# Optimization experiments

Measured on AMD Instinct MI355X. Metric: run time of the kernel, lower is better.

Reference implementation:

```python
import itertools
import jax, jax.numpy as jnp
import numpy as np

N1 = 4
N2 = 4
D = 3
BATCH = 512
NDENSE = 256
FEAT_IN = (N1 + N2) * D  # 24


def _perms_and_signs(n):
    P = np.array(list(itertools.permutations(range(n))), dtype=np.int32)  # [n!, n], lexicographic
    # sign = (-1)^(number of inversions)
    triu = np.triu(np.ones((n, n), dtype=np.int64), 1)
    inv = np.sum((P[:, :, None] > P[:, None, :]) * triu, axis=(1, 2))
    signs = np.where(inv % 2 == 0, 1.0, -1.0).astype(np.float32)
    return P, signs

P1_np, S1_np = _perms_and_signs(N1)
P2_np, S2_np = _perms_and_signs(N2)


def setup_inputs() -> dict:
    key = jax.random.key(0)
    ks = jax.random.split(key, 12)
    def dense_init(k, fan_in, fan_out):
        return jax.random.normal(k, (fan_in, fan_out), jnp.float32) / jnp.sqrt(jnp.float32(fan_in))
    inp = {
        "x1": jax.random.normal(ks[0], (BATCH, N1, D), jnp.float32),
        "x2": jax.random.normal(ks[1], (BATCH, N2, D), jnp.float32),
        "W0": dense_init(ks[2], FEAT_IN, NDENSE),
        "b0": jnp.zeros((NDENSE,), jnp.float32),
        "W1": dense_init(ks[3], NDENSE, NDENSE),
        "b1": jnp.zeros((NDENSE,), jnp.float32),
        "W2": dense_init(ks[4], NDENSE, NDENSE),
        "b2": jnp.zeros((NDENSE,), jnp.float32),
        "Wf": dense_init(ks[5], NDENSE, 1),
        "bf": jnp.zeros((1,), jnp.float32),
    }
    return inp


def _resnet(h, W0, b0, W1, b1, W2, b2, Wf, bf):
    # SimpleResNet: residual tanh dense layers (skip when shapes match), linear head
    y = jnp.tanh(h @ W0 + b0)            # [.., 24] -> [.., 256]: no skip (shape mismatch)
    y = jnp.tanh(y @ W1 + b1) + y        # residual
    y = jnp.tanh(y @ W2 + b2) + y        # residual
    return y @ Wf + bf                   # [.., 1], no activation


def reference(x1, x2, W0, b0, W1, b1, W2, b2, Wf, bf):
    P1 = jnp.asarray(P1_np); P2 = jnp.asarray(P2_np)
    s1 = jnp.asarray(S1_np); s2 = jnp.asarray(S2_np)
    nf1, nf2 = P1.shape[0], P2.shape[0]  # 24, 24
    # all permutations along particle axis
    p1 = jnp.take(x1, P1, axis=-2)       # [B, nf1, n1, d]
    p2 = jnp.take(x2, P2, axis=-2)       # [B, nf2, n2, d]
    # broadcast to cross product of permutation axes
    b1_ = jnp.broadcast_to(p1[:, :, None, :, :], (x1.shape[0], nf1, nf2, N1, D))
    b2_ = jnp.broadcast_to(p2[:, None, :, :, :], (x2.shape[0], nf1, nf2, N2, D))
    concat = jnp.concatenate([b1_, b2_], axis=-2)                  # [B, nf1, nf2, n1+n2, d]
    feats = concat.reshape(concat.shape[:-2] + (-1,))              # [B, nf1, nf2, (n1+n2)*d]
    out = _resnet(feats, W0, b0, W1, b1, W2, b2, Wf, bf)           # [B, nf1, nf2, 1]
    signed = out * s1[:, None, None] * s2[:, None]                 # sign-weighted
    anti = jnp.sum(signed, axis=(-1, -2, -3))                      # [B]
    return jnp.log(jnp.abs(anti))
```

## Files before the change

kernel.cpp:

```cpp
#include <hip/hip_runtime.h>
#include <math.h>

#define NPERM 24
#define ND 256
#define RPB 48
#define RPW 12
#define ROWS_PER_B 576
#define BATCH 512
#define TOTAL_ROWS (BATCH * ROWS_PER_B)
#define NBLOCKS (TOTAL_ROWS / RPB)

__constant__ int c_P[NPERM * 4] = {
    0,1,2,3, 0,1,3,2, 0,2,1,3, 0,2,3,1, 0,3,1,2, 0,3,2,1,
    1,0,2,3, 1,0,3,2, 1,2,0,3, 1,2,3,0, 1,3,0,2, 1,3,2,0,
    2,0,1,3, 2,0,3,1, 2,1,0,3, 2,1,3,0, 2,3,0,1, 2,3,1,0,
    3,0,1,2, 3,0,2,1, 3,1,0,2, 3,1,2,0, 3,2,0,1, 3,2,1,0
};
__constant__ float c_S[NPERM] = {
     1.f,-1.f,-1.f, 1.f, 1.f,-1.f,
    -1.f, 1.f, 1.f,-1.f,-1.f, 1.f,
     1.f,-1.f,-1.f, 1.f, 1.f,-1.f,
    -1.f, 1.f, 1.f,-1.f,-1.f, 1.f
};

__global__ __launch_bounds__(256, 2)
void fused_resnet(const float* __restrict__ x1, const float* __restrict__ x2,
                  const float* __restrict__ W0, const float* __restrict__ b0,
                  const float* __restrict__ W1, const float* __restrict__ b1,
                  const float* __restrict__ W2, const float* __restrict__ b2,
                  const float* __restrict__ Wf, const float* __restrict__ bf,
                  double* __restrict__ anti)
{
    __shared__ float sY[RPB * ND];
    __shared__ float sStage[4096];
    const int t   = threadIdx.x;
    const int tc  = t & 63;
    const int tr  = t >> 6;
    const int gr0 = blockIdx.x * RPB;
    const int b   = gr0 / ROWS_PER_B;

    for (int e = t; e < RPB * 24; e += 256) {
        int lr = e / 24, c = e % 24;
        int pp = (gr0 + lr) % ROWS_PER_B;
        float v;
        if (c < 12) {
            int p1 = pp / 24;
            v = x1[b * 12 + c_P[p1 * 4 + c / 3] * 3 + (c % 3)];
        } else {
            int p2 = pp % 24; int cc = c - 12;
            v = x2[b * 12 + c_P[p2 * 4 + cc / 3] * 3 + (cc % 3)];
        }
        sStage[2048 + e] = v;
    }

    float acc[RPW][4];

    #pragma unroll
    for (int r = 0; r < RPW; ++r) { acc[r][0]=0.f; acc[r][1]=0.f; acc[r][2]=0.f; acc[r][3]=0.f; }
    for (int kt = 0; kt < 24; kt += 8) {
        __syncthreads();
        {
            const float4* src = (const float4*)(W0 + kt * ND);
            float4* dst = (float4*)sStage;
            for (int i = t; i < (8 * ND) / 4; i += 256) dst[i] = src[i];
        }
        __syncthreads();
        #pragma unroll
        for (int k4 = 0; k4 < 2; ++k4) {
            float w[4][4];
            #pragma unroll
            for (int k = 0; k < 4; ++k) {
                float4 wv = *(const float4*)&sStage[(k4 * 4 + k) * ND + 4 * tc];
                w[k][0]=wv.x; w[k][1]=wv.y; w[k][2]=wv.z; w[k][3]=wv.w;
            }
            #pragma unroll
            for (int r = 0; r < RPW; ++r) {
                float4 yv = *(const float4*)&sStage[2048 + (tr * RPW + r) * 24 + kt + k4 * 4];
                float yk[4] = {yv.x, yv.y, yv.z, yv.w};
                #pragma unroll
                for (int k = 0; k < 4; ++k)
                    #pragma unroll
                    for (int c = 0; c < 4; ++c)
                        acc[r][c] = fmaf(yk[k], w[k][c], acc[r][c]);
            }
        }
    }
    {
        float4 bv = *(const float4*)&b0[4 * tc];
        float bb[4] = {bv.x, bv.y, bv.z, bv.w};
        __syncthreads();
        #pragma unroll
        for (int r = 0; r < RPW; ++r) {
            float4 o;
            o.x = tanhf(acc[r][0] + bb[0]);
            o.y = tanhf(acc[r][1] + bb[1]);
            o.z = tanhf(acc[r][2] + bb[2]);
            o.w = tanhf(acc[r][3] + bb[3]);
            *(float4*)&sY[(tr * RPW + r) * ND + 4 * tc] = o;
        }
        __syncthreads();
    }

    #pragma unroll 1
    for (int layer = 0; layer < 2; ++layer) {
        const float* W   = layer ? W2 : W1;
        const float* bbp = layer ? b2 : b1;
        #pragma unroll
        for (int r = 0; r < RPW; ++r) { acc[r][0]=0.f; acc[r][1]=0.f; acc[r][2]=0.f; acc[r][3]=0.f; }
        for (int kt = 0; kt < ND; kt += 16) {
            __syncthreads();
            {
                const float4* src = (const float4*)(W + kt * ND);
                float4* dst = (float4*)sStage;
                #pragma unroll
                for (int i = 0; i < 4; ++i) dst[t + i * 256] = src[t + i * 256];
            }
            __syncthreads();
            #pragma unroll
            for (int k4 = 0; k4 < 4; ++k4) {
                float w[4][4];
                #pragma unroll
                for (int k = 0; k < 4; ++k) {
                    float4 wv = *(const float4*)&sStage[(k4 * 4 + k) * ND + 4 * tc];
                    w[k][0]=wv.x; w[k][1]=wv.y; w[k][2]=wv.z; w[k][3]=wv.w;
                }
                #pragma unroll
                for (int r = 0; r < RPW; ++r) {
                    float4 yv = *(const float4*)&sY[(tr * RPW + r) * ND + kt + k4 * 4];
                    float yk[4] = {yv.x, yv.y, yv.z, yv.w};
                    #pragma unroll
                    for (int k = 0; k < 4; ++k)
                        #pragma unroll
                        for (int c = 0; c < 4; ++c)
                            acc[r][c] = fmaf(yk[k], w[k][c], acc[r][c]);
                }
            }
        }
        float4 bv = *(const float4*)&bbp[4 * tc];
        float bb[4] = {bv.x, bv.y, bv.z, bv.w};
        float ny[RPW][4];
        #pragma unroll
        for (int r = 0; r < RPW; ++r) {
            float4 yo = *(const float4*)&sY[(tr * RPW + r) * ND + 4 * tc];
            float yov[4] = {yo.x, yo.y, yo.z, yo.w};
            #pragma unroll
            for (int c = 0; c < 4; ++c)
                ny[r][c] = tanhf(acc[r][c] + bb[c]) + yov[c];
        }
        __syncthreads();
        #pragma unroll
        for (int r = 0; r < RPW; ++r) {
            float4 o; o.x = ny[r][0]; o.y = ny[r][1]; o.z = ny[r][2]; o.w = ny[r][3];
            *(float4*)&sY[(tr * RPW + r) * ND + 4 * tc] = o;
        }
        __syncthreads();
    }

    if (t < 64) {
        ((float4*)sStage)[t] = ((const float4*)Wf)[t];
    }
    __syncthreads();
    double contrib = 0.0;
    if (tc < RPW) {
        int row = tr * RPW + tc;
        const float* yrow = &sY[row * ND];
        float f = 0.f;
        #pragma unroll 8
        for (int k = 0; k < ND; ++k) f = fmaf(yrow[k], sStage[k], f);
        f += bf[0];
        int pp = (gr0 + row) % ROWS_PER_B;
        double s = (double)(c_S[pp / 24] * c_S[pp % 24]);
        contrib = s * (double)f;
    }
    #pragma unroll
    for (int off = 32; off > 0; off >>= 1) contrib += __shfl_xor(contrib, off, 64);
    if (tc == 0) atomicAdd(&anti[b], contrib);
}

__global__ void finalize_log(const double* __restrict__ anti, float* __restrict__ out) {
    int i = blockIdx.x * 256 + threadIdx.x;
    if (i < BATCH) out[i] = (float)log(fabs(anti[i]));
}

extern "C" void kernel_launch(void* const* d_in, const int* in_sizes, int n_in,
                              void* d_out, int out_size, void* d_ws, size_t ws_size,
                              hipStream_t stream) {
    const float* x1 = (const float*)d_in[0];
    const float* x2 = (const float*)d_in[1];
    const float* W0 = (const float*)d_in[2];
    const float* b0 = (const float*)d_in[3];
    const float* W1 = (const float*)d_in[4];
    const float* b1 = (const float*)d_in[5];
    const float* W2 = (const float*)d_in[6];
    const float* b2 = (const float*)d_in[7];
    const float* Wf = (const float*)d_in[8];
    const float* bf = (const float*)d_in[9];
    double* anti = (double*)d_ws;
    float* out   = (float*)d_out;

    hipMemsetAsync(anti, 0, BATCH * sizeof(double), stream);
    fused_resnet<<<NBLOCKS, 256, 0, stream>>>(x1, x2, W0, b0, W1, b1, W2, b2, Wf, bf, anti);
    finalize_log<<<(BATCH + 255) / 256, 256, 0, stream>>>(anti, out);
}
```

Before: 1.295 ms.

## Double-buffer weight tiles in LDS using async global_load_lds prefetch

```diff
diff --git a/kernel.cpp b/kernel.cpp
--- a/kernel.cpp
+++ b/kernel.cpp
@@ -7,8 +7,7 @@
 #define RPW 12
 #define ROWS_PER_B 576
 #define BATCH 512
-#define TOTAL_ROWS (BATCH * ROWS_PER_B)
-#define NBLOCKS (TOTAL_ROWS / RPB)
+#define NBLOCKS (BATCH * ROWS_PER_B / RPB)
 
 __constant__ int c_P[NPERM * 4] = {
     0,1,2,3, 0,1,3,2, 0,2,1,3, 0,2,3,1, 0,3,1,2, 0,3,2,1,
@@ -23,6 +22,12 @@
     -1.f, 1.f, 1.f,-1.f,-1.f, 1.f
 };
 
+__device__ __forceinline__ void gl_lds16(const float* g, float* l) {
+    __builtin_amdgcn_global_load_lds(
+        (const __attribute__((address_space(1))) void*)g,
+        (__attribute__((address_space(3)))  void*)l, 16, 0, 0);
+}
+
 __global__ __launch_bounds__(256, 2)
 void fused_resnet(const float* __restrict__ x1, const float* __restrict__ x2,
                   const float* __restrict__ W0, const float* __restrict__ b0,
@@ -32,12 +37,18 @@
                   double* __restrict__ anti)
 {
     __shared__ float sY[RPB * ND];
-    __shared__ float sStage[4096];
+    __shared__ float sW[8192];
     const int t   = threadIdx.x;
     const int tc  = t & 63;
     const int tr  = t >> 6;
     const int gr0 = blockIdx.x * RPB;
     const int b   = gr0 / ROWS_PER_B;
+
+    #pragma unroll
+    for (int i = 0; i < 2; ++i) {
+        int c = tr * 2 + i;
+        gl_lds16(W0 + c * 256 + tc * 4, &sW[c * 256]);
+    }
 
     for (int e = t; e < RPB * 24; e += 256) {
         int lr = e / 24, c = e % 24;
@@ -50,32 +61,36 @@
             int p2 = pp % 24; int cc = c - 12;
             v = x2[b * 12 + c_P[p2 * 4 + cc / 3] * 3 + (cc % 3)];
         }
-        sStage[2048 + e] = v;
+        sW[4096 + e] = v;
     }
 
     float acc[RPW][4];
 
     #pragma unroll
     for (int r = 0; r < RPW; ++r) { acc[r][0]=0.f; acc[r][1]=0.f; acc[r][2]=0.f; acc[r][3]=0.f; }
-    for (int kt = 0; kt < 24; kt += 8) {
+    for (int kt3 = 0; kt3 < 3; ++kt3) {
         __syncthreads();
-        {
-            const float4* src = (const float4*)(W0 + kt * ND);
-            float4* dst = (float4*)sStage;
-            for (int i = t; i < (8 * ND) / 4; i += 256) dst[i] = src[i];
-        }
-        __syncthreads();
+        if (kt3 < 2) {
+            const float* src = W0 + (kt3 + 1) * 2048;
+            float* dst = &sW[((kt3 + 1) & 1) * 2048];
+            #pragma unroll
+            for (int i = 0; i < 2; ++i) {
+                int c = tr * 2 + i;
+                gl_lds16(src + c * 256 + tc * 4, dst + c * 256);
+            }
+        }
+        const float* wt = &sW[(kt3 & 1) * 2048];
         #pragma unroll
         for (int k4 = 0; k4 < 2; ++k4) {
             float w[4][4];
             #pragma unroll
             for (int k = 0; k < 4; ++k) {
-                float4 wv = *(const float4*)&sStage[(k4 * 4 + k) * ND + 4 * tc];
+                float4 wv = *(const float4*)&wt[(k4 * 4 + k) * 256 + 4 * tc];
                 w[k][0]=wv.x; w[k][1]=wv.y; w[k][2]=wv.z; w[k][3]=wv.w;
             }
             #pragma unroll
             for (int r = 0; r < RPW; ++r) {
-                float4 yv = *(const float4*)&sStage[2048 + (tr * RPW + r) * 24 + kt + k4 * 4];
+                float4 yv = *(const float4*)&sW[4096 + (tr * RPW + r) * 24 + kt3 * 8 + k4 * 4];
                 float yk[4] = {yv.x, yv.y, yv.z, yv.w};
                 #pragma unroll
                 for (int k = 0; k < 4; ++k)
@@ -85,10 +100,15 @@
             }
         }
     }
+    __syncthreads();
+    #pragma unroll
+    for (int i = 0; i < 4; ++i) {
+        int c = tr * 4 + i;
+        gl_lds16(W1 + c * 256 + tc * 4, &sW[4096 + c * 256]);
+    }
     {
         float4 bv = *(const float4*)&b0[4 * tc];
         float bb[4] = {bv.x, bv.y, bv.z, bv.w};
-        __syncthreads();
         #pragma unroll
         for (int r = 0; r < RPW; ++r) {
             float4 o;
@@ -98,35 +118,47 @@
             o.w = tanhf(acc[r][3] + bb[3]);
             *(float4*)&sY[(tr * RPW + r) * ND + 4 * tc] = o;
         }
-        __syncthreads();
-    }
-
+    }
+
+    int cur = 1;
     #pragma unroll 1
     for (int layer = 0; layer < 2; ++layer) {
-        const float* W   = layer ? W2 : W1;
-        const float* bbp = layer ? b2 : b1;
+        const float* Wcur = layer ? W2 : W1;
+        const float* bcur = layer ? b2 : b1;
         #pragma unroll
         for (int r = 0; r < RPW; ++r) { acc[r][0]=0.f; acc[r][1]=0.f; acc[r][2]=0.f; acc[r][3]=0.f; }
-        for (int kt = 0; kt < ND; kt += 16) {
+        #pragma unroll 1
+        for (int ktile = 0; ktile < 16; ++ktile) {
             __syncthreads();
-            {
-                const float4* src = (const float4*)(W + kt * ND);
-                float4* dst = (float4*)sStage;
-                #pragma unroll
-                for (int i = 0; i < 4; ++i) dst[t + i * 256] = src[t + i * 256];
-            }
-            __syncthreads();
+            float* nb = &sW[(1 - cur) * 4096];
+            if (ktile < 15) {
+                const float* src = Wcur + (ktile + 1) * 4096;
+                #pragma unroll
+                for (int i = 0; i < 4; ++i) {
+                    int c = tr * 4 + i;
+                    gl_lds16(src + c * 256 + tc * 4, nb + c * 256);
+                }
+            } else if (layer == 0) {
+                #pragma unroll
+                for (int i = 0; i < 4; ++i) {
+                    int c = tr * 4 + i;
+                    gl_lds16(W2 + c * 256 + tc * 4, nb + c * 256);
+                }
+            } else {
+                gl_lds16(Wf + tc * 4, nb + tr * 256);
+            }
+            const float* wt = &sW[cur * 4096];
             #pragma unroll
             for (int k4 = 0; k4 < 4; ++k4) {
                 float w[4][4];
                 #pragma unroll
                 for (int k = 0; k < 4; ++k) {
-                    float4 wv = *(const float4*)&sStage[(k4 * 4 + k) * ND + 4 * tc];
+                    float4 wv = *(const float4*)&wt[(k4 * 4 + k) * 256 + 4 * tc];
                     w[k][0]=wv.x; w[k][1]=wv.y; w[k][2]=wv.z; w[k][3]=wv.w;
                 }
                 #pragma unroll
                 for (int r = 0; r < RPW; ++r) {
-                    float4 yv = *(const float4*)&sY[(tr * RPW + r) * ND + kt + k4 * 4];
+                    float4 yv = *(const float4*)&sY[(tr * RPW + r) * ND + ktile * 16 + k4 * 4];
                     float yk[4] = {yv.x, yv.y, yv.z, yv.w};
                     #pragma unroll
                     for (int k = 0; k < 4; ++k)
@@ -135,38 +167,31 @@
                             acc[r][c] = fmaf(yk[k], w[k][c], acc[r][c]);
                 }
             }
-        }
-        float4 bv = *(const float4*)&bbp[4 * tc];
+            cur ^= 1;
+        }
+        float4 bv = *(const float4*)&bcur[4 * tc];
         float bb[4] = {bv.x, bv.y, bv.z, bv.w};
-        float ny[RPW][4];
         #pragma unroll
         for (int r = 0; r < RPW; ++r) {
             float4 yo = *(const float4*)&sY[(tr * RPW + r) * ND + 4 * tc];
-            float yov[4] = {yo.x, yo.y, yo.z, yo.w};
-            #pragma unroll
-            for (int c = 0; c < 4; ++c)
-                ny[r][c] = tanhf(acc[r][c] + bb[c]) + yov[c];
-        }
-        __syncthreads();
-        #pragma unroll
-        for (int r = 0; r < RPW; ++r) {
-            float4 o; o.x = ny[r][0]; o.y = ny[r][1]; o.z = ny[r][2]; o.w = ny[r][3];
+            float4 o;
+            o.x = tanhf(acc[r][0] + bb[0]) + yo.x;
+            o.y = tanhf(acc[r][1] + bb[1]) + yo.y;
+            o.z = tanhf(acc[r][2] + bb[2]) + yo.z;
+            o.w = tanhf(acc[r][3] + bb[3]) + yo.w;
             *(float4*)&sY[(tr * RPW + r) * ND + 4 * tc] = o;
         }
-        __syncthreads();
-    }
-
-    if (t < 64) {
-        ((float4*)sStage)[t] = ((const float4*)Wf)[t];
-    }
+    }
+
     __syncthreads();
     double contrib = 0.0;
     if (tc < RPW) {
         int row = tr * RPW + tc;
         const float* yrow = &sY[row * ND];
+        const float* wfp  = &sW[4096 + tr * 256];
         float f = 0.f;
         #pragma unroll 8
-        for (int k = 0; k < ND; ++k) f = fmaf(yrow[k], sStage[k], f);
+        for (int k = 0; k < ND; ++k) f = fmaf(yrow[k], wfp[k], f);
         f += bf[0];
         int pp = (gr0 + row) % ROWS_PER_B;
         double s = (double)(c_S[pp / 24] * c_S[pp % 24]);
```

Result: slower. 1.483 ms (+14.5%).

## Assign one row per lane with wave-uniform weight columns read via scalar loads

Applied to the files above, without the earlier changes.

```diff
diff --git a/kernel.cpp b/kernel.cpp
--- a/kernel.cpp
+++ b/kernel.cpp
@@ -1,22 +1,20 @@
 #include <hip/hip_runtime.h>
 #include <math.h>
 
-#define NPERM 24
 #define ND 256
-#define RPB 48
-#define RPW 12
+#define RPB 64
 #define ROWS_PER_B 576
 #define BATCH 512
-#define TOTAL_ROWS (BATCH * ROWS_PER_B)
-#define NBLOCKS (TOTAL_ROWS / RPB)
+#define BPE 9
+#define NBLOCKS (BATCH * BPE)
 
-__constant__ int c_P[NPERM * 4] = {
+__constant__ int c_P[24 * 4] = {
     0,1,2,3, 0,1,3,2, 0,2,1,3, 0,2,3,1, 0,3,1,2, 0,3,2,1,
     1,0,2,3, 1,0,3,2, 1,2,0,3, 1,2,3,0, 1,3,0,2, 1,3,2,0,
     2,0,1,3, 2,0,3,1, 2,1,0,3, 2,1,3,0, 2,3,0,1, 2,3,1,0,
     3,0,1,2, 3,0,2,1, 3,1,0,2, 3,1,2,0, 3,2,0,1, 3,2,1,0
 };
-__constant__ float c_S[NPERM] = {
+__constant__ float c_S[24] = {
      1.f,-1.f,-1.f, 1.f, 1.f,-1.f,
     -1.f, 1.f, 1.f,-1.f,-1.f, 1.f,
      1.f,-1.f,-1.f, 1.f, 1.f,-1.f,
@@ -31,150 +29,76 @@
                   const float* __restrict__ Wf, const float* __restrict__ bf,
                   double* __restrict__ anti)
 {
-    __shared__ float sY[RPB * ND];
-    __shared__ float sStage[4096];
-    const int t   = threadIdx.x;
-    const int tc  = t & 63;
-    const int tr  = t >> 6;
-    const int gr0 = blockIdx.x * RPB;
-    const int b   = gr0 / ROWS_PER_B;
+    __shared__ float sYT[ND * RPB];
+    const int t    = threadIdx.x;
+    const int lane = t & 63;
+    const int wid  = t >> 6;
+    const int cb   = __builtin_amdgcn_readfirstlane(wid << 6);
+    const int b    = blockIdx.x / BPE;
+    const int pp   = (blockIdx.x % BPE) * RPB + lane;
+    const int p1   = pp / 24, p2 = pp % 24;
 
-    for (int e = t; e < RPB * 24; e += 256) {
-        int lr = e / 24, c = e % 24;
-        int pp = (gr0 + lr) % ROWS_PER_B;
-        float v;
-        if (c < 12) {
-            int p1 = pp / 24;
-            v = x1[b * 12 + c_P[p1 * 4 + c / 3] * 3 + (c % 3)];
-        } else {
-            int p2 = pp % 24; int cc = c - 12;
-            v = x2[b * 12 + c_P[p2 * 4 + cc / 3] * 3 + (cc % 3)];
+    float feats[24];
+    #pragma unroll
+    for (int i = 0; i < 4; ++i)
+        #pragma unroll
+        for (int d = 0; d < 3; ++d) {
+            feats[i * 3 + d]      = x1[b * 12 + c_P[p1 * 4 + i] * 3 + d];
+            feats[12 + i * 3 + d] = x2[b * 12 + c_P[p2 * 4 + i] * 3 + d];
         }
-        sStage[2048 + e] = v;
-    }
 
-    float acc[RPW][4];
+    float acc[64], yprev[64];
 
     #pragma unroll
-    for (int r = 0; r < RPW; ++r) { acc[r][0]=0.f; acc[r][1]=0.f; acc[r][2]=0.f; acc[r][3]=0.f; }
-    for (int kt = 0; kt < 24; kt += 8) {
-        __syncthreads();
-        {
-            const float4* src = (const float4*)(W0 + kt * ND);
-            float4* dst = (float4*)sStage;
-            for (int i = t; i < (8 * ND) / 4; i += 256) dst[i] = src[i];
+    for (int j = 0; j < 64; ++j) acc[j] = 0.f;
+    #pragma unroll 1
+    for (int k = 0; k < 24; ++k) {
+        const float* wk = W0 + k * ND + cb;
+        float yk = feats[k];
+        #pragma unroll
+        for (int j = 0; j < 64; ++j) acc[j] = fmaf(yk, wk[j], acc[j]);
+    }
+    #pragma unroll
+    for (int j = 0; j < 64; ++j) {
+        yprev[j] = tanhf(acc[j] + b0[cb + j]);
+        sYT[(cb + j) * RPB + lane] = yprev[j];
+    }
+    __syncthreads();
+
+    #pragma unroll 1
+    for (int layer = 0; layer < 2; ++layer) {
+        const float* W  = layer ? W2 : W1;
+        const float* bb = layer ? b2 : b1;
+        #pragma unroll
+        for (int j = 0; j < 64; ++j) acc[j] = 0.f;
+        #pragma unroll 2
+        for (int k = 0; k < ND; ++k) {
+            float yk = sYT[k * RPB + lane];
+            const float* wk = W + k * ND + cb;
+            #pragma unroll
+            for (int j = 0; j < 64; ++j) acc[j] = fmaf(yk, wk[j], acc[j]);
         }
         __syncthreads();
         #pragma unroll
-        for (int k4 = 0; k4 < 2; ++k4) {
-            float w[4][4];
-            #pragma unroll
-            for (int k = 0; k < 4; ++k) {
-                float4 wv = *(const float4*)&sStage[(k4 * 4 + k) * ND + 4 * tc];
-                w[k][0]=wv.x; w[k][1]=wv.y; w[k][2]=wv.z; w[k][3]=wv.w;
-            }
-            #pragma unroll
-            for (int r = 0; r < RPW; ++r) {
-                float4 yv = *(const float4*)&sStage[2048 + (tr * RPW + r) * 24 + kt + k4 * 4];
-                float yk[4] = {yv.x, yv.y, yv.z, yv.w};
-                #pragma unroll
-                for (int k = 0; k < 4; ++k)
-                    #pragma unroll
-                    for (int c = 0; c < 4; ++c)
-                        acc[r][c] = fmaf(yk[k], w[k][c], acc[r][c]);
-            }
-        }
-    }
-    {
-        float4 bv = *(const float4*)&b0[4 * tc];
-        float bb[4] = {bv.x, bv.y, bv.z, bv.w};
-        __syncthreads();
-        #pragma unroll
-        for (int r = 0; r < RPW; ++r) {
-            float4 o;
-            o.x = tanhf(acc[r][0] + bb[0]);
-            o.y = tanhf(acc[r][1] + bb[1]);
-            o.z = tanhf(acc[r][2] + bb[2]);
-            o.w = tanhf(acc[r][3] + bb[3]);
-            *(float4*)&sY[(tr * RPW + r) * ND + 4 * tc] = o;
+        for (int j = 0; j < 64; ++j) {
+            float ny = tanhf(acc[j] + bb[cb + j]) + yprev[j];
+            yprev[j] = ny;
+            sYT[(cb + j) * RPB + lane] = ny;
         }
         __syncthreads();
     }
 
-    #pragma unroll 1
-    for (int layer = 0; layer < 2; ++layer) {
-        const float* W   = layer ? W2 : W1;
-        const float* bbp = layer ? b2 : b1;
+    if (wid == 0) {
+        float f = 0.f;
+        #pragma unroll 1
+        for (int k = 0; k < ND; ++k)
+            f = fmaf(sYT[k * RPB + lane], Wf[k], f);
+        f += bf[0];
+        double contrib = (double)(c_S[p1] * c_S[p2]) * (double)f;
         #pragma unroll
-        for (int r = 0; r < RPW; ++r) { acc[r][0]=0.f; acc[r][1]=0.f; acc[r][2]=0.f; acc[r][3]=0.f; }
-        for (int kt = 0; kt < ND; kt += 16) {
-            __syncthreads();
-            {
-                const float4* src = (const float4*)(W + kt * ND);
-                float4* dst = (float4*)sStage;
-                #pragma unroll
-                for (int i = 0; i < 4; ++i) dst[t + i * 256] = src[t + i * 256];
-            }
-            __syncthreads();
-            #pragma unroll
-            for (int k4 = 0; k4 < 4; ++k4) {
-                float w[4][4];
-                #pragma unroll
-                for (int k = 0; k < 4; ++k) {
-                    float4 wv = *(const float4*)&sStage[(k4 * 4 + k) * ND + 4 * tc];
-                    w[k][0]=wv.x; w[k][1]=wv.y; w[k][2]=wv.z; w[k][3]=wv.w;
-                }
-                #pragma unroll
-                for (int r = 0; r < RPW; ++r) {
-                    float4 yv = *(const float4*)&sY[(tr * RPW + r) * ND + kt + k4 * 4];
-                    float yk[4] = {yv.x, yv.y, yv.z, yv.w};
-                    #pragma unroll
-                    for (int k = 0; k < 4; ++k)
-                        #pragma unroll
-                        for (int c = 0; c < 4; ++c)
-                            acc[r][c] = fmaf(yk[k], w[k][c], acc[r][c]);
-                }
-            }
-        }
-        float4 bv = *(const float4*)&bbp[4 * tc];
-        float bb[4] = {bv.x, bv.y, bv.z, bv.w};
-        float ny[RPW][4];
-        #pragma unroll
-        for (int r = 0; r < RPW; ++r) {
-            float4 yo = *(const float4*)&sY[(tr * RPW + r) * ND + 4 * tc];
-            float yov[4] = {yo.x, yo.y, yo.z, yo.w};
-            #pragma unroll
-            for (int c = 0; c < 4; ++c)
-                ny[r][c] = tanhf(acc[r][c] + bb[c]) + yov[c];
-        }
-        __syncthreads();
-        #pragma unroll
-        for (int r = 0; r < RPW; ++r) {
-            float4 o; o.x = ny[r][0]; o.y = ny[r][1]; o.z = ny[r][2]; o.w = ny[r][3];
-            *(float4*)&sY[(tr * RPW + r) * ND + 4 * tc] = o;
-        }
-        __syncthreads();
+        for (int off = 32; off > 0; off >>= 1) contrib += __shfl_xor(contrib, off, 64);
+        if (lane == 0) atomicAdd(&anti[b], contrib);
     }
-
-    if (t < 64) {
-        ((float4*)sStage)[t] = ((const float4*)Wf)[t];
-    }
-    __syncthreads();
-    double contrib = 0.0;
-    if (tc < RPW) {
-        int row = tr * RPW + tc;
-        const float* yrow = &sY[row * ND];
-        float f = 0.f;
-        #pragma unroll 8
-        for (int k = 0; k < ND; ++k) f = fmaf(yrow[k], sStage[k], f);
-        f += bf[0];
-        int pp = (gr0 + row) % ROWS_PER_B;
-        double s = (double)(c_S[pp / 24] * c_S[pp % 24]);
-        contrib = s * (double)f;
-    }
-    #pragma unroll
-    for (int off = 32; off > 0; off >>= 1) contrib += __shfl_xor(contrib, off, 64);
-    if (tc == 0) atomicAdd(&anti[b], contrib);
 }
 
 __global__ void finalize_log(const double* __restrict__ anti, float* __restrict__ out) {
```

Result: slower. 2.584 ms (+99.5%).
